# Performance work log

Hardware: AMD Instinct MI355X
Metric: run time of the kernel (lower is better)

Reference implementation:

```python
import jax, jax.numpy as jnp
import numpy as np

EPS = 1e-5

def _ln(x):
    m = jnp.mean(x, axis=-1, keepdims=True)
    v = jnp.mean((x - m) ** 2, axis=-1, keepdims=True)
    return (x - m) / jnp.sqrt(v + EPS)

def setup_inputs() -> dict:
    key = jax.random.key(0)
    ks = jax.random.split(key, 6)
    B, S, E, H = 2, 2048, 1024, 16
    sd = 1.0 / np.sqrt(E)
    x = jax.random.normal(ks[0], (B, S, E), dtype=jnp.float32)
    w_in = jax.random.normal(ks[1], (3 * E, E), dtype=jnp.float32) * sd
    w_out = jax.random.normal(ks[2], (E, E), dtype=jnp.float32) * sd
    w_fc = jax.random.normal(ks[3], (4 * E, E), dtype=jnp.float32) * sd
    b_fc = jnp.zeros((4 * E,), dtype=jnp.float32)
    w_proj = jax.random.normal(ks[4], (E, 4 * E), dtype=jnp.float32) * (1.0 / np.sqrt(4 * E))
    b_proj = jnp.zeros((E,), dtype=jnp.float32)
    return {"x": x, "w_in": w_in, "w_out": w_out, "w_fc": w_fc,
            "b_fc": b_fc, "w_proj": w_proj, "b_proj": b_proj}

def reference(x, w_in, w_out, w_fc, b_fc, w_proj, b_proj):
    B, S, E = x.shape
    H = 16
    D = E // H
    h = _ln(x)
    qkv = h @ w_in.T                      # [B,S,3E]
    q, k, v = jnp.split(qkv, 3, axis=-1)
    q = q.reshape(B, S, H, D)
    k = k.reshape(B, S, H, D)
    v = v.reshape(B, S, H, D)
    scale = 1.0 / np.sqrt(D)
    scores = jnp.einsum('bqhd,bkhd->bhqk', q, k) * scale  # [B,H,S,S]
    causal = jnp.tril(jnp.ones((S, S), dtype=bool))
    scores = jnp.where(causal, scores, -jnp.inf)
    attn = jax.nn.softmax(scores, axis=-1)
    o = jnp.einsum('bhqk,bkhd->bqhd', attn, v).reshape(B, S, E)
    attn_out = o @ w_out.T
    x2 = x + attn_out                      # residual 1
    h2 = _ln(x2)
    m = jax.nn.relu(h2 @ w_fc.T + b_fc)    # [B,S,4E]
    return (m @ w_proj.T + b_proj) + x2    # residual 2
```

## Files before the change

### kernel.cpp

```cpp
#include <hip/hip_runtime.h>
#include <stdint.h>

#define AS1 __attribute__((address_space(1)))
#define AS3 __attribute__((address_space(3)))

typedef __bf16 bf8_t __attribute__((ext_vector_type(8)));
typedef float f4_t __attribute__((ext_vector_type(4)));
typedef unsigned short ush;

__device__ __forceinline__ ush f2b(float f) {
  unsigned u = __builtin_bit_cast(unsigned, f);
  u += 0x7fffu + ((u >> 16) & 1u);
  return (ush)(u >> 16);
}
__device__ __forceinline__ void unpack8(uint4 u, float* dst) {
  unsigned a0 = u.x, a1 = u.y, a2 = u.z, a3 = u.w;
  dst[0] = __builtin_bit_cast(float, a0 << 16);
  dst[1] = __builtin_bit_cast(float, a0 & 0xffff0000u);
  dst[2] = __builtin_bit_cast(float, a1 << 16);
  dst[3] = __builtin_bit_cast(float, a1 & 0xffff0000u);
  dst[4] = __builtin_bit_cast(float, a2 << 16);
  dst[5] = __builtin_bit_cast(float, a2 & 0xffff0000u);
  dst[6] = __builtin_bit_cast(float, a3 << 16);
  dst[7] = __builtin_bit_cast(float, a3 & 0xffff0000u);
}

__global__ __launch_bounds__(256) void f2b_all(
    const float* __restrict__ w_in, const float* __restrict__ w_out,
    const float* __restrict__ w_fc, const float* __restrict__ w_proj,
    ush* __restrict__ o_in, ush* __restrict__ o_out,
    ush* __restrict__ o_fc, ush* __restrict__ o_proj) {
  const int blk = blockIdx.x;
  const float* src;
  ush* dst;
  int base;
  if (blk < 3072) { src = w_in; dst = o_in; base = blk; }
  else if (blk < 4096) { src = w_out; dst = o_out; base = blk - 3072; }
  else if (blk < 8192) { src = w_fc; dst = o_fc; base = blk - 4096; }
  else { src = w_proj; dst = o_proj; base = blk - 8192; }
  const int i = (base * 256 + threadIdx.x) * 4;
  float4 v = *(const float4*)(src + i);
  union { ush u[4]; uint2 d; } p;
  p.u[0] = f2b(v.x); p.u[1] = f2b(v.y); p.u[2] = f2b(v.z); p.u[3] = f2b(v.w);
  *(uint2*)(dst + i) = p.d;
}

__global__ __launch_bounds__(256) void ln_kernel(const float* __restrict__ x,
                                                 ush* __restrict__ out) {
  const int row = blockIdx.x, tid = threadIdx.x;
  const float* xr = x + (size_t)row * 1024;
  float4 v = ((const float4*)xr)[tid];
  float s = v.x + v.y + v.z + v.w;
  float q = v.x * v.x + v.y * v.y + v.z * v.z + v.w * v.w;
  for (int o = 32; o; o >>= 1) { s += __shfl_down(s, o); q += __shfl_down(q, o); }
  __shared__ float rs[4], rq[4];
  const int w = tid >> 6;
  if ((tid & 63) == 0) { rs[w] = s; rq[w] = q; }
  __syncthreads();
  s = rs[0] + rs[1] + rs[2] + rs[3];
  q = rq[0] + rq[1] + rq[2] + rq[3];
  const float mean = s * (1.0f / 1024.0f);
  const float var = q * (1.0f / 1024.0f) - mean * mean;
  const float rstd = rsqrtf(var + 1e-5f);
  union { ush u[4]; uint2 d; } p;
  p.u[0] = f2b((v.x - mean) * rstd);
  p.u[1] = f2b((v.y - mean) * rstd);
  p.u[2] = f2b((v.z - mean) * rstd);
  p.u[3] = f2b((v.w - mean) * rstd);
  *(uint2*)(out + (size_t)row * 1024 + tid * 4) = p.d;
}

template <int EPI>
__global__ __launch_bounds__(512, 2) void gemm8p(
    const ush* __restrict__ A, const ush* __restrict__ Bw,
    int M, int N, int K, int lda, int ldb,
    const float* __restrict__ bias, const float* __restrict__ resid,
    float* __restrict__ outF, ush* __restrict__ outB) {
  __shared__ __align__(16) ush lds[65536];
  ush* const LA0 = lds;
  ush* const LA1 = lds + 16384;
  ush* const LB0 = lds + 32768;
  ush* const LB1 = lds + 49152;

  const int tid = threadIdx.x;
  const int wave = tid >> 6, lane = tid & 63;
  const int wm = wave >> 2, wn = wave & 3;
  const int l16 = lane & 15, quad = lane >> 4;
  const int sw = l16 & 7;
  const int bm = blockIdx.x, bn = blockIdx.y;
  const int bmrow = bm * 256, bnrow = bn * 256;
  const size_t kbase = (size_t)blockIdx.z * (size_t)K;
  const int KT = K >> 6;
  const int nit = KT >> 1;
  const int gcs = (((lane & 7) ^ ((lane >> 3) & 7)) << 3);

  auto stage = [&](const ush* __restrict__ gbase, int blkrow, int ld,
                   ush* dstbase, int t, int h) {
    const int kt = t & (KT - 1);
#pragma unroll
    for (int i2 = 0; i2 < 2; ++i2) {
      const int rr = h * 128 + (wave * 2 + i2) * 8 + (lane >> 3);
      const ush* g = gbase + (size_t)(blkrow + rr) * ld + kbase + kt * 64 + gcs;
      __builtin_amdgcn_global_load_lds(
          (const AS1 void*)g,
          (AS3 void*)(dstbase + h * 8192 + (wave * 2 + i2) * 512), 16, 0, 0);
    }
  };

  f4_t acc[8][4];
#pragma unroll
  for (int i = 0; i < 8; ++i)
#pragma unroll
    for (int j = 0; j < 4; ++j) acc[i][j] = (f4_t){0.f, 0.f, 0.f, 0.f};

  stage(A, bmrow, lda, LA0, 0, 0);
  stage(A, bmrow, lda, LA0, 0, 1);
  stage(Bw, bnrow, ldb, LB0, 0, 0);
  stage(Bw, bnrow, ldb, LB0, 0, 1);
  stage(A, bmrow, lda, LA1, 1, 0);
  asm volatile("s_waitcnt vmcnt(2)" ::: "memory");
  __builtin_amdgcn_s_barrier();

  bf8_t af[4][2], bf[2][2];

  for (int it = 0; it < nit; ++it) {
#pragma unroll
    for (int hf = 0; hf < 2; ++hf) {
      ush* const cA = hf ? LA1 : LA0;
      ush* const cB = hf ? LB1 : LB0;
#pragma unroll
      for (int sub = 0; sub < 4; ++sub) {
        const int p = hf * 4 + sub;
        if (sub == 0) {
#pragma unroll
          for (int m = 0; m < 4; ++m)
#pragma unroll
            for (int kk = 0; kk < 2; ++kk)
              af[m][kk] = *(const bf8_t*)&cA[(wm * 128 + m * 16 + l16) * 64 +
                                            (((kk * 4 + quad) ^ sw) << 3)];
#pragma unroll
          for (int n = 0; n < 2; ++n)
#pragma unroll
            for (int kk = 0; kk < 2; ++kk)
              bf[n][kk] = *(const bf8_t*)&cB[(wn * 64 + n * 16 + l16) * 64 +
                                            (((kk * 4 + quad) ^ sw) << 3)];
        } else if (sub == 1) {
#pragma unroll
          for (int n = 0; n < 2; ++n)
#pragma unroll
            for (int kk = 0; kk < 2; ++kk)
              bf[n][kk] = *(const bf8_t*)&cB[(wn * 64 + (2 + n) * 16 + l16) * 64 +
                                            (((kk * 4 + quad) ^ sw) << 3)];
        } else if (sub == 2) {
#pragma unroll
          for (int m = 0; m < 4; ++m)
#pragma unroll
            for (int kk = 0; kk < 2; ++kk)
              af[m][kk] = *(const bf8_t*)&cA[(wm * 128 + (4 + m) * 16 + l16) * 64 +
                                            (((kk * 4 + quad) ^ sw) << 3)];
#pragma unroll
          for (int n = 0; n < 2; ++n)
#pragma unroll
            for (int kk = 0; kk < 2; ++kk)
              bf[n][kk] = *(const bf8_t*)&cB[(wn * 64 + n * 16 + l16) * 64 +
                                            (((kk * 4 + quad) ^ sw) << 3)];
        } else {
#pragma unroll
          for (int n = 0; n < 2; ++n)
#pragma unroll
            for (int kk = 0; kk < 2; ++kk)
              bf[n][kk] = *(const bf8_t*)&cB[(wn * 64 + (2 + n) * 16 + l16) * 64 +
                                            (((kk * 4 + quad) ^ sw) << 3)];
        }
        if (p == 0) stage(A, bmrow, lda, LA1, 2 * it + 1, 1);
        else if (p == 1) stage(Bw, bnrow, ldb, LB1, 2 * it + 1, 0);
        else if (p == 2) stage(Bw, bnrow, ldb, LB1, 2 * it + 1, 1);
        else if (p == 3) stage(A, bmrow, lda, LA0, 2 * it + 2, 0);
        else if (p == 4) stage(A, bmrow, lda, LA0, 2 * it + 2, 1);
        else if (p == 5) stage(Bw, bnrow, ldb, LB0, 2 * it + 2, 0);
        else if (p == 6) stage(Bw, bnrow, ldb, LB0, 2 * it + 2, 1);
        else stage(A, bmrow, lda, LA1, 2 * it + 3, 0);
        if (sub == 3) asm volatile("s_waitcnt vmcnt(2)" ::: "memory");
        __builtin_amdgcn_s_barrier();
        asm volatile("s_waitcnt lgkmcnt(0)" ::: "memory");
        __builtin_amdgcn_sched_barrier(0);
        __builtin_amdgcn_s_setprio(1);
        const int mo = (sub >= 2) ? 4 : 0;
        const int no = (sub & 1) ? 2 : 0;
#pragma unroll
        for (int m = 0; m < 4; ++m)
#pragma unroll
          for (int n = 0; n < 2; ++n)
#pragma unroll
            for (int kk = 0; kk < 2; ++kk)
              acc[mo + m][no + n] = __builtin_amdgcn_mfma_f32_16x16x32_bf16(
                  af[m][kk], bf[n][kk], acc[mo + m][no + n], 0, 0, 0);
        __builtin_amdgcn_s_setprio(0);
        __builtin_amdgcn_s_barrier();
      }
    }
  }

  asm volatile("s_waitcnt vmcnt(0)" ::: "memory");
  __builtin_amdgcn_s_barrier();

  if (EPI == 0 || EPI == 2) {
    ush* outBz = outB + (size_t)blockIdx.z * ((size_t)M * N);
    ush* eb = lds + wave * 8192;
    float bv[4];
    if (EPI == 2) {
#pragma unroll
      for (int ni = 0; ni < 4; ++ni) bv[ni] = bias[bn * 256 + wn * 64 + ni * 16 + l16];
    }
#pragma unroll
    for (int mi = 0; mi < 8; ++mi)
#pragma unroll
      for (int ni = 0; ni < 4; ++ni)
#pragma unroll
        for (int r = 0; r < 4; ++r) {
          float v = acc[mi][ni][r];
          if (EPI == 2) v = fmaxf(v + bv[ni], 0.0f);
          eb[(mi * 16 + quad * 4 + r) * 64 + ni * 16 + l16] = f2b(v);
        }
    asm volatile("s_waitcnt lgkmcnt(0)" ::: "memory");
#pragma unroll
    for (int j = 0; j < 16; ++j) {
      const int lr = j * 8 + (lane >> 3);
      const int c8 = (lane & 7) * 8;
      uint4 v = *(const uint4*)&eb[lr * 64 + c8];
      *(uint4*)(outBz + (size_t)(bm * 256 + wm * 128 + lr) * N + bn * 256 +
                wn * 64 + c8) = v;
    }
  } else {
#pragma unroll
    for (int mi = 0; mi < 8; ++mi)
#pragma unroll
      for (int ni = 0; ni < 4; ++ni) {
        const int gm0 = bm * 256 + wm * 128 + mi * 16 + quad * 4;
        const int gn = bn * 256 + wn * 64 + ni * 16 + l16;
        const float bv = (EPI == 3) ? bias[gn] : 0.0f;
#pragma unroll
        for (int r = 0; r < 4; ++r) {
          const size_t idx = (size_t)(gm0 + r) * N + gn;
          outF[idx] = acc[mi][ni][r] + bv + resid[idx];
        }
      }
  }
}

__global__ __launch_bounds__(256) void reduce4(const ush* __restrict__ p,
                                               const float* __restrict__ bias,
                                               const float* __restrict__ resid,
                                               float* __restrict__ out) {
  const size_t i = ((size_t)blockIdx.x * 256 + threadIdx.x) * 8;
  const int col = (int)(i & 1023);
  float acc[8];
  float4 r0 = *(const float4*)(resid + i);
  float4 r1 = *(const float4*)(resid + i + 4);
  acc[0] = r0.x + bias[col + 0]; acc[1] = r0.y + bias[col + 1];
  acc[2] = r0.z + bias[col + 2]; acc[3] = r0.w + bias[col + 3];
  acc[4] = r1.x + bias[col + 4]; acc[5] = r1.y + bias[col + 5];
  acc[6] = r1.z + bias[col + 6]; acc[7] = r1.w + bias[col + 7];
#pragma unroll
  for (int z = 0; z < 4; ++z) {
    uint4 u = *(const uint4*)(p + (size_t)z * 4194304 + i);
    float f[8]; unpack8(u, f);
#pragma unroll
    for (int j = 0; j < 8; ++j) acc[j] += f[j];
  }
  *(float4*)(out + i) = *(float4*)acc;
  *(float4*)(out + i + 4) = *(float4*)(acc + 4);
}

template <int EPI, int BM, int MINW>
__global__ __launch_bounds__(256, MINW) void gemm_bt(
    const ush* __restrict__ A, const ush* __restrict__ Bw,
    int M, int N, int K,
    const float* __restrict__ bias, const float* __restrict__ resid,
    float* __restrict__ outF, ush* __restrict__ outB) {
  constexpr int MI = BM / 32;
  constexpr int NCH = (BM + 128) / 16;
  constexpr int PC = NCH / 4;
  constexpr int ASZ = BM * 32;
  __shared__ ush lds[2 * ASZ + 2 * 4096];
  const int tid = threadIdx.x;
  const int wave = tid >> 6, lane = tid & 63;
  const int bm = blockIdx.x, bn = blockIdx.y;
  const int wm = (wave & 1) * (BM / 2), wn = (wave >> 1) * 64;
  const int l16 = lane & 15, quad = lane >> 4;
  const int srow = lane >> 2;
  const int scol = (lane & 3) * 8;

  const ush* Abase = A + (size_t)(bm * BM) * K;
  const ush* Bbase = Bw + (size_t)(bn * 128) * K;

  f4_t acc[MI][4];
#pragma unroll
  for (int i = 0; i < MI; ++i)
#pragma unroll
    for (int j = 0; j < 4; ++j) acc[i][j] = (f4_t){0.f, 0.f, 0.f, 0.f};

  const int kiters = K >> 5;

  auto stage = [&](int k0, int buf) {
    const int kk = k0 * 32;
#pragma unroll
    for (int i = 0; i < PC; ++i) {
      const int c = wave * PC + i;
      if (c < BM / 16) {
        const ush* ga = Abase + (size_t)(c * 16 + srow) * K + kk + scol;
        __builtin_amdgcn_global_load_lds((const AS1 void*)ga,
                                         (AS3 void*)(lds + buf * ASZ + c * 512), 16, 0, 0);
      } else {
        const int c2 = c - BM / 16;
        const ush* gb = Bbase + (size_t)(c2 * 16 + srow) * K + kk + scol;
        __builtin_amdgcn_global_load_lds(
            (const AS1 void*)gb, (AS3 void*)(lds + 2 * ASZ + buf * 4096 + c2 * 512), 16, 0, 0);
      }
    }
  };

  stage(0, 0);
  __syncthreads();
  for (int k0 = 0; k0 < kiters; ++k0) {
    const int cur = k0 & 1;
    if (k0 + 1 < kiters) stage(k0 + 1, cur ^ 1);
    bf8_t af[MI], bfr[4];
#pragma unroll
    for (int mi = 0; mi < MI; ++mi)
      af[mi] = *(const bf8_t*)&lds[cur * ASZ + (wm + mi * 16 + l16) * 32 + quad * 8];
#pragma unroll
    for (int ni = 0; ni < 4; ++ni)
      bfr[ni] = *(const bf8_t*)&lds[2 * ASZ + cur * 4096 + (wn + ni * 16 + l16) * 32 + quad * 8];
#pragma unroll
    for (int mi = 0; mi < MI; ++mi)
#pragma unroll
      for (int ni = 0; ni < 4; ++ni)
        acc[mi][ni] =
            __builtin_amdgcn_mfma_f32_16x16x32_bf16(af[mi], bfr[ni], acc[mi][ni], 0, 0, 0);
    __syncthreads();
  }

  if (EPI == 0 || EPI == 2) {
    ush* eb = lds + wave * ASZ;
#pragma unroll
    for (int mi = 0; mi < MI; ++mi)
#pragma unroll
      for (int ni = 0; ni < 4; ++ni) {
        const int gn = bn * 128 + wn + ni * 16 + l16;
        const float bv = (EPI == 2) ? bias[gn] : 0.0f;
#pragma unroll
        for (int r = 0; r < 4; ++r) {
          float v = acc[mi][ni][r] + bv;
          if (EPI == 2) v = fmaxf(v, 0.0f);
          eb[(mi * 16 + quad * 4 + r) * 64 + ni * 16 + l16] = f2b(v);
        }
      }
#pragma unroll
    for (int j = 0; j < BM / 16; ++j) {
      const int lr = j * 8 + (lane >> 3);
      const int c8 = (lane & 7) * 8;
      uint4 v = *(const uint4*)&eb[lr * 64 + c8];
      *(uint4*)(outB + (size_t)(bm * BM + wm + lr) * N + bn * 128 + wn + c8) = v;
    }
  } else {
#pragma unroll
    for (int mi = 0; mi < MI; ++mi) {
#pragma unroll
      for (int ni = 0; ni < 4; ++ni) {
        const int gm0 = bm * BM + wm + mi * 16 + quad * 4;
        const int gn = bn * 128 + wn + ni * 16 + l16;
        const float bv = (EPI == 3) ? bias[gn] : 0.0f;
#pragma unroll
        for (int r = 0; r < 4; ++r) {
          const size_t idx = (size_t)(gm0 + r) * N + gn;
          outF[idx] = acc[mi][ni][r] + bv + resid[idx];
        }
      }
    }
  }
}

__global__ __launch_bounds__(256) void pack_kv(const ush* __restrict__ qkv,
                                               ush* __restrict__ Kp,
                                               ush* __restrict__ Vp) {
  const int lin = blockIdx.x;
  const int kt = lin & 31, h = (lin >> 5) & 15, b = lin >> 9;
  const int tid = threadIdx.x;
  __shared__ ush Vs[64 * 72];
  const size_t rowbase = (size_t)(b * 2048 + kt * 64) * 3072 + h * 64;
  ush* Kt = Kp + (size_t)lin * 4096;
  ush* Vt = Vp + (size_t)lin * 4096;

  const int r0 = tid >> 3, cin = tid & 7;
#pragma unroll
  for (int it = 0; it < 2; ++it) {
    const int r = r0 + it * 32;
    uint4 ku = *(const uint4*)(qkv + rowbase + (size_t)r * 3072 + 1024 + cin * 8);
    float f[8]; unpack8(ku, f);
    union { ush us[8]; uint4 v; } pk;
#pragma unroll
    for (int j = 0; j < 8; ++j) pk.us[j] = f2b(f[j] * 0.125f);
    *(uint4*)(Kt + (size_t)(r * 8 + (cin ^ (r & 7))) * 8) = pk.v;
    uint4 vu = *(const uint4*)(qkv + rowbase + (size_t)r * 3072 + 2048 + cin * 8);
    *(uint4*)&Vs[r * 72 + cin * 8] = vu;
  }
  __syncthreads();
#pragma unroll
  for (int oc2 = 0; oc2 < 2; ++oc2) {
    const int oc = tid * 2 + oc2;
    const int d = oc >> 3, c = oc & 7;
    const int k0 = 8 * (c ^ (d & 7));
    union { ush us[8]; uint4 v; } pk;
#pragma unroll
    for (int j = 0; j < 8; ++j) pk.us[j] = Vs[(k0 + j) * 72 + d];
    *(uint4*)(Vt + (size_t)oc * 8) = pk.v;
  }
}

__global__ __launch_bounds__(256, 4) void attn_kernel(const ush* __restrict__ qkv,
                                                      const ush* __restrict__ Kp,
                                                      const ush* __restrict__ Vp,
                                                      ush* __restrict__ o) {
  const int lin = blockIdx.x;
  const int b = lin & 1, h = (lin >> 1) & 15, tq = lin >> 5;
  const int tid = threadIdx.x;
  const int wave = tid >> 6, lane = tid & 63;
  const int l15 = lane & 15, quad = lane >> 4;

  __shared__ __align__(16) ush Ks[64 * 64];
  __shared__ __align__(16) ush Vt[64 * 64];
  __shared__ __align__(16) ush Ps[64 * 72];

  bf8_t qf[2];
  {
    const int qrow = b * 2048 + tq * 64 + wave * 16 + l15;
#pragma unroll
    for (int s = 0; s < 2; ++s) {
      union { uint4 u; bf8_t v; } pk;
      pk.u = *(const uint4*)(qkv + (size_t)qrow * 3072 + h * 64 + s * 32 + quad * 8);
      qf[s] = pk.v;
    }
  }

  float m_s = -1e30f, l_s = 0.f;
  f4_t O[4];
#pragma unroll
  for (int j = 0; j < 4; ++j) O[j] = (f4_t){0.f, 0.f, 0.f, 0.f};

  const int qw0 = tq * 64 + wave * 16;
  const int swz = (l15 & 7) * 8;
  const size_t tile0 = (size_t)((b * 16 + h) * 32) * 4096;

  for (int kt = 0; kt <= tq; ++kt) {
    __syncthreads();
    const ush* Ktile = Kp + tile0 + (size_t)kt * 4096;
    const ush* Vtile = Vp + tile0 + (size_t)kt * 4096;
#pragma unroll
    for (int i = 0; i < 2; ++i) {
      const int seg = wave * 2 + i;
      __builtin_amdgcn_global_load_lds((const AS1 void*)(Ktile + seg * 512 + lane * 8),
                                       (AS3 void*)(Ks + seg * 512), 16, 0, 0);
      __builtin_amdgcn_global_load_lds((const AS1 void*)(Vtile + seg * 512 + lane * 8),
                                       (AS3 void*)(Vt + seg * 512), 16, 0, 0);
    }
    __syncthreads();

    f4_t S[4];
#pragma unroll
    for (int mi = 0; mi < 4; ++mi) S[mi] = (f4_t){0.f, 0.f, 0.f, 0.f};
#pragma unroll
    for (int s = 0; s < 2; ++s)
#pragma unroll
      for (int mi = 0; mi < 4; ++mi) {
        bf8_t kf = *(const bf8_t*)&Ks[(mi * 16 + l15) * 64 + (((4 * s + quad) * 8) ^ swz)];
        S[mi] = __builtin_amdgcn_mfma_f32_16x16x32_bf16(kf, qf[s], S[mi], 0, 0, 0);
      }

    if (kt == tq) {
#pragma unroll
      for (int mi = 0; mi < 4; ++mi)
#pragma unroll
        for (int r = 0; r < 4; ++r) {
          const int kg = kt * 64 + mi * 16 + quad * 4 + r;
          const int qg = qw0 + l15;
          if (kg > qg) S[mi][r] = -1e30f;
        }
    }

    float mx = -1e30f;
#pragma unroll
    for (int mi = 0; mi < 4; ++mi)
#pragma unroll
      for (int r = 0; r < 4; ++r) mx = fmaxf(mx, S[mi][r]);
    mx = fmaxf(mx, __shfl_xor(mx, 16));
    mx = fmaxf(mx, __shfl_xor(mx, 32));
    const float mn = fmaxf(m_s, mx);
    const float alpha = __expf(m_s - mn);
    float sum = 0.f;
#pragma unroll
    for (int mi = 0; mi < 4; ++mi)
#pragma unroll
      for (int r = 0; r < 4; ++r) {
        const float p = __expf(S[mi][r] - mn);
        S[mi][r] = p;
        sum += p;
      }
    sum += __shfl_xor(sum, 16);
    sum += __shfl_xor(sum, 32);
    m_s = mn;
    l_s = l_s * alpha + sum;
#pragma unroll
    for (int mi = 0; mi < 4; ++mi) {
      uint2 w2;
      w2.x = (unsigned)f2b(S[mi][0]) | ((unsigned)f2b(S[mi][1]) << 16);
      w2.y = (unsigned)f2b(S[mi][2]) | ((unsigned)f2b(S[mi][3]) << 16);
      *(uint2*)&Ps[(wave * 16 + l15) * 72 + mi * 16 + quad * 4] = w2;
    }

    bf8_t pf[2], vf[4][2];
#pragma unroll
    for (int s = 0; s < 2; ++s)
      pf[s] = *(const bf8_t*)&Ps[(wave * 16 + l15) * 72 + s * 32 + quad * 8];
#pragma unroll
    for (int n4 = 0; n4 < 4; ++n4)
#pragma unroll
      for (int s = 0; s < 2; ++s)
        vf[n4][s] = *(const bf8_t*)&Vt[(n4 * 16 + l15) * 64 + (((4 * s + quad) * 8) ^ swz)];
    float ar[4];
#pragma unroll
    for (int r = 0; r < 4; ++r) ar[r] = __shfl(alpha, quad * 4 + r);
#pragma unroll
    for (int n4 = 0; n4 < 4; ++n4) {
#pragma unroll
      for (int r = 0; r < 4; ++r) O[n4][r] *= ar[r];
#pragma unroll
      for (int s = 0; s < 2; ++s)
        O[n4] = __builtin_amdgcn_mfma_f32_16x16x32_bf16(pf[s], vf[n4][s], O[n4], 0, 0, 0);
    }
  }

  const float rc = 1.0f / l_s;
  float rr[4];
#pragma unroll
  for (int r = 0; r < 4; ++r) rr[r] = __shfl(rc, quad * 4 + r);
#pragma unroll
  for (int n4 = 0; n4 < 4; ++n4)
#pragma unroll
    for (int r = 0; r < 4; ++r) {
      const int qg = tq * 64 + wave * 16 + quad * 4 + r;
      o[(size_t)(b * 2048 + qg) * 1024 + h * 64 + n4 * 16 + l15] = f2b(O[n4][r] * rr[r]);
    }
}

extern "C" void kernel_launch(void* const* d_in, const int* in_sizes, int n_in,
                              void* d_out, int out_size, void* d_ws, size_t ws_size,
                              hipStream_t stream) {
  const float* x = (const float*)d_in[0];
  const float* w_in = (const float*)d_in[1];
  const float* w_out = (const float*)d_in[2];
  const float* w_fc = (const float*)d_in[3];
  const float* b_fc = (const float*)d_in[4];
  const float* w_proj = (const float*)d_in[5];
  const float* b_proj = (const float*)d_in[6];
  float* out = (float*)d_out;

  char* ws = (char*)d_ws;
  ush* w_in_b = (ush*)(ws);
  ush* w_out_b = (ush*)(ws + 6291456);
  ush* h_b = (ush*)(ws + 8388608);
  ush* Kp = (ush*)(ws + 16777216);
  ush* Vp = (ush*)(ws + 25165824);
  ush* Pp = (ush*)(ws);
  ush* w_fc_b = (ush*)(ws + 33554432);
  ush* w_proj_b = (ush*)(ws + 41943040);
  float* x2 = (float*)(ws + 50331648);
  ush* qkv_b = (ush*)(ws + 67108864);
  ush* m_b = (ush*)(ws + 67108864);
  ush* o_b = (ush*)(ws + 92274688);

  f2b_all<<<12288, 256, 0, stream>>>(w_in, w_out, w_fc, w_proj,
                                     w_in_b, w_out_b, w_fc_b, w_proj_b);

  ln_kernel<<<4096, 256, 0, stream>>>(x, h_b);

  gemm8p<0><<<dim3(16, 12), 512, 0, stream>>>(
      h_b, w_in_b, 4096, 3072, 1024, 1024, 1024, nullptr, nullptr, nullptr, qkv_b);

  pack_kv<<<1024, 256, 0, stream>>>(qkv_b, Kp, Vp);

  attn_kernel<<<1024, 256, 0, stream>>>(qkv_b, Kp, Vp, o_b);

  gemm_bt<1, 64, 4><<<dim3(64, 8), 256, 0, stream>>>(
      o_b, w_out_b, 4096, 1024, 1024, nullptr, x, x2, nullptr);

  ln_kernel<<<4096, 256, 0, stream>>>(x2, h_b);

  gemm8p<2><<<dim3(16, 16), 512, 0, stream>>>(
      h_b, w_fc_b, 4096, 4096, 1024, 1024, 1024, b_fc, nullptr, nullptr, m_b);

  gemm8p<0><<<dim3(16, 4, 4), 512, 0, stream>>>(
      m_b, w_proj_b, 4096, 1024, 1024, 4096, 4096, nullptr, nullptr, nullptr, Pp);

  reduce4<<<2048, 256, 0, stream>>>(Pp, b_proj, x2, out);
}
```

Baseline: 310.2 us.

## Double-buffer K/V tiles, use exp2 with lazy rescale, reverse causal tile order

The attention kernel now double-buffers K/V tiles in LDS and prefetches the next tile with global_load_lds while computing on the current one, so there is one barrier per iteration instead of two. The K prescale folds in log2(e) so softmax can use the raw v_exp_f32 (exp2) instruction, and the running-max rescale of O and l is skipped unless the max grows by more than 8. Query tiles are scheduled heaviest-first to reduce tail imbalance. P is packed with v_cvt_pk_bf16_f32. The lazy rescale allows unnormalised exponentials up to 2^8, which is safe in fp32 but slightly changes bf16 rounding of P. Doubling the K/V buffers also raises LDS use per block.

```diff
diff --git a/kernel.cpp b/kernel.cpp
--- a/kernel.cpp
+++ b/kernel.cpp
@@ -400,7 +400,7 @@
     float f[8]; unpack8(ku, f);
     union { ush us[8]; uint4 v; } pk;
 #pragma unroll
-    for (int j = 0; j < 8; ++j) pk.us[j] = f2b(f[j] * 0.125f);
+    for (int j = 0; j < 8; ++j) pk.us[j] = f2b(f[j] * 0.18033688f);
     *(uint4*)(Kt + (size_t)(r * 8 + (cin ^ (r & 7))) * 8) = pk.v;
     uint4 vu = *(const uint4*)(qkv + rowbase + (size_t)r * 3072 + 2048 + cin * 8);
     *(uint4*)&Vs[r * 72 + cin * 8] = vu;
@@ -423,13 +423,13 @@
                                                       const ush* __restrict__ Vp,
                                                       ush* __restrict__ o) {
   const int lin = blockIdx.x;
-  const int b = lin & 1, h = (lin >> 1) & 15, tq = lin >> 5;
+  const int b = lin & 1, h = (lin >> 1) & 15, tq = 31 - (lin >> 5);
   const int tid = threadIdx.x;
   const int wave = tid >> 6, lane = tid & 63;
   const int l15 = lane & 15, quad = lane >> 4;
 
-  __shared__ __align__(16) ush Ks[64 * 64];
-  __shared__ __align__(16) ush Vt[64 * 64];
+  __shared__ __align__(16) ush Ks[2 * 4096];
+  __shared__ __align__(16) ush Vt[2 * 4096];
   __shared__ __align__(16) ush Ps[64 * 72];
 
   bf8_t qf[2];
@@ -452,10 +452,9 @@
   const int swz = (l15 & 7) * 8;
   const size_t tile0 = (size_t)((b * 16 + h) * 32) * 4096;
 
-  for (int kt = 0; kt <= tq; ++kt) {
-    __syncthreads();
-    const ush* Ktile = Kp + tile0 + (size_t)kt * 4096;
-    const ush* Vtile = Vp + tile0 + (size_t)kt * 4096;
+  {
+    const ush* Ktile = Kp + tile0;
+    const ush* Vtile = Vp + tile0;
 #pragma unroll
     for (int i = 0; i < 2; ++i) {
       const int seg = wave * 2 + i;
@@ -464,7 +463,25 @@
       __builtin_amdgcn_global_load_lds((const AS1 void*)(Vtile + seg * 512 + lane * 8),
                                        (AS3 void*)(Vt + seg * 512), 16, 0, 0);
     }
-    __syncthreads();
+  }
+  asm volatile("s_waitcnt vmcnt(0)" ::: "memory");
+  __builtin_amdgcn_s_barrier();
+
+  for (int kt = 0; kt <= tq; ++kt) {
+    const int cur = (kt & 1) * 4096;
+    const int nxt = 4096 - cur;
+    if (kt < tq) {
+      const ush* Ktile = Kp + tile0 + (size_t)(kt + 1) * 4096;
+      const ush* Vtile = Vp + tile0 + (size_t)(kt + 1) * 4096;
+#pragma unroll
+      for (int i = 0; i < 2; ++i) {
+        const int seg = wave * 2 + i;
+        __builtin_amdgcn_global_load_lds((const AS1 void*)(Ktile + seg * 512 + lane * 8),
+                                         (AS3 void*)(Ks + nxt + seg * 512), 16, 0, 0);
+        __builtin_amdgcn_global_load_lds((const AS1 void*)(Vtile + seg * 512 + lane * 8),
+                                         (AS3 void*)(Vt + nxt + seg * 512), 16, 0, 0);
+      }
+    }
 
     f4_t S[4];
 #pragma unroll
@@ -473,7 +490,7 @@
     for (int s = 0; s < 2; ++s)
 #pragma unroll
       for (int mi = 0; mi < 4; ++mi) {
-        bf8_t kf = *(const bf8_t*)&Ks[(mi * 16 + l15) * 64 + (((4 * s + quad) * 8) ^ swz)];
+        bf8_t kf = *(const bf8_t*)&Ks[cur + (mi * 16 + l15) * 64 + (((4 * s + quad) * 8) ^ swz)];
         S[mi] = __builtin_amdgcn_mfma_f32_16x16x32_bf16(kf, qf[s], S[mi], 0, 0, 0);
       }
 
@@ -495,26 +512,43 @@
       for (int r = 0; r < 4; ++r) mx = fmaxf(mx, S[mi][r]);
     mx = fmaxf(mx, __shfl_xor(mx, 16));
     mx = fmaxf(mx, __shfl_xor(mx, 32));
-    const float mn = fmaxf(m_s, mx);
-    const float alpha = __expf(m_s - mn);
+
+    if (!__all(mx - m_s <= 8.0f)) {
+      const float mn = fmaxf(m_s, mx);
+      const float dm = m_s - mn;
+      float alpha;
+      asm("v_exp_f32 %0, %1" : "=v"(alpha) : "v"(dm));
+      float ar[4];
+#pragma unroll
+      for (int r = 0; r < 4; ++r) ar[r] = __shfl(alpha, quad * 4 + r);
+#pragma unroll
+      for (int n4 = 0; n4 < 4; ++n4)
+#pragma unroll
+        for (int r = 0; r < 4; ++r) O[n4][r] *= ar[r];
+      l_s *= alpha;
+      m_s = mn;
+    }
+
     float sum = 0.f;
 #pragma unroll
     for (int mi = 0; mi < 4; ++mi)
 #pragma unroll
       for (int r = 0; r < 4; ++r) {
-        const float p = __expf(S[mi][r] - mn);
-        S[mi][r] = p;
-        sum += p;
+        const float z = S[mi][r] - m_s;
+        float pv;
+        asm("v_exp_f32 %0, %1" : "=v"(pv) : "v"(z));
+        S[mi][r] = pv;
+        sum += pv;
       }
     sum += __shfl_xor(sum, 16);
     sum += __shfl_xor(sum, 32);
-    m_s = mn;
-    l_s = l_s * alpha + sum;
+    l_s += sum;
+
 #pragma unroll
     for (int mi = 0; mi < 4; ++mi) {
       uint2 w2;
-      w2.x = (unsigned)f2b(S[mi][0]) | ((unsigned)f2b(S[mi][1]) << 16);
-      w2.y = (unsigned)f2b(S[mi][2]) | ((unsigned)f2b(S[mi][3]) << 16);
+      asm("v_cvt_pk_bf16_f32 %0, %1, %2" : "=v"(w2.x) : "v"(S[mi][0]), "v"(S[mi][1]));
+      asm("v_cvt_pk_bf16_f32 %0, %1, %2" : "=v"(w2.y) : "v"(S[mi][2]), "v"(S[mi][3]));
       *(uint2*)&Ps[(wave * 16 + l15) * 72 + mi * 16 + quad * 4] = w2;
     }
 
@@ -526,18 +560,15 @@
     for (int n4 = 0; n4 < 4; ++n4)
 #pragma unroll
       for (int s = 0; s < 2; ++s)
-        vf[n4][s] = *(const bf8_t*)&Vt[(n4 * 16 + l15) * 64 + (((4 * s + quad) * 8) ^ swz)];
-    float ar[4];
-#pragma unroll
-    for (int r = 0; r < 4; ++r) ar[r] = __shfl(alpha, quad * 4 + r);
-#pragma unroll
-    for (int n4 = 0; n4 < 4; ++n4) {
-#pragma unroll
-      for (int r = 0; r < 4; ++r) O[n4][r] *= ar[r];
+        vf[n4][s] = *(const bf8_t*)&Vt[cur + (n4 * 16 + l15) * 64 + (((4 * s + quad) * 8) ^ swz)];
+#pragma unroll
+    for (int n4 = 0; n4 < 4; ++n4)
 #pragma unroll
       for (int s = 0; s < 2; ++s)
         O[n4] = __builtin_amdgcn_mfma_f32_16x16x32_bf16(pf[s], vf[n4][s], O[n4], 0, 0, 0);
-    }
+
+    asm volatile("s_waitcnt vmcnt(0)" ::: "memory");
+    __builtin_amdgcn_s_barrier();
   }
 
   const float rc = 1.0f / l_s;
```

New measurement: 303.5 us. 1.02x faster.
